# Kernel optimization log

Measured on AMD Instinct MI355X. Metric: run time of the kernel, lower is better.

The kernel has to match this reference:

```python
import jax, jax.numpy as jnp
import numpy as np

B, S, HID = 2, 2048, 2048
NH, NKV, HD = 16, 16, 128
SCALE = 1.0 / np.sqrt(HD)


def _rotate_half(x):
    x1, x2 = jnp.split(x, 2, axis=-1)
    return jnp.concatenate([-x2, x1], axis=-1)


def setup_inputs() -> dict:
    key = jax.random.key(0)
    k1, k2, k3 = jax.random.split(key, 3)
    hidden_states = jax.random.normal(k1, (B, S, HID), dtype=jnp.float32)
    # standard RoPE cos/sin tables, shape [S, HD]
    inv_freq = 1.0 / (10000.0 ** (np.arange(0, HD, 2, dtype=np.float32) / HD))
    freqs = np.outer(np.arange(S, dtype=np.float32), inv_freq)  # [S, HD/2]
    emb = np.concatenate([freqs, freqs], axis=-1)               # [S, HD]
    cos = jnp.asarray(np.cos(emb), dtype=jnp.float32)
    sin = jnp.asarray(np.sin(emb), dtype=jnp.float32)
    # torch Linear weights are [out, in]; forward computes x @ W.T
    w_qkv = jax.random.normal(k2, ((NH + 2 * NKV) * HD, HID), dtype=jnp.float32) * 0.02
    w_o = jax.random.normal(k3, (HID, NH * HD), dtype=jnp.float32) * 0.02
    return {"hidden_states": hidden_states, "cos": cos, "sin": sin,
            "w_qkv": w_qkv, "w_o": w_o}


def reference(hidden_states, cos, sin, w_qkv, w_o):
    b, s, _ = hidden_states.shape
    qkv = hidden_states @ w_qkv.T                         # [B,S,(NH+2*NKV)*HD]
    qkv = qkv.reshape(b, s, NH + 2 * NKV, HD)
    q = qkv[:, :, :NH]                                    # [B,S,NH,HD]
    k = qkv[:, :, NH:NH + NKV]                            # [B,S,NKV,HD]
    v = qkv[:, :, NH + NKV:]                              # [B,S,NKV,HD]
    # RoPE: broadcast cos/sin [S,HD] -> [1,S,1,HD]
    c = cos[None, :, None, :]
    sn = sin[None, :, None, :]
    q = q * c + _rotate_half(q) * sn
    k = k * c + _rotate_half(k) * sn
    scores = jnp.einsum("bihd,bjhd->bhij", q, k) * SCALE  # [B,H,S,S]
    attn = jax.nn.softmax(scores, axis=-1)
    out = jnp.einsum("bhij,bjhd->bihd", attn, v)          # [B,S,H,HD]
    out = out.reshape(b, s, NH * HD)
    return out @ w_o.T                                    # [B,S,HID]
```

## Files before the change

kernel.cpp:

```cpp
#include <hip/hip_runtime.h>
#include <hip/hip_bf16.h>

typedef float f32x4 __attribute__((ext_vector_type(4)));
typedef __bf16 bf16x8 __attribute__((ext_vector_type(8)));
typedef __bf16 bf16x4 __attribute__((ext_vector_type(4)));

#define S_LEN 2048
#define NHEADS 16
#define HDIM 128
#define KLOG2E (0.08838834764831845f * 1.4426950408889634f)
#define MSHIFT 2.0f

__device__ __forceinline__ void gld_lds16(const __bf16* g, __bf16* l) {
  __builtin_amdgcn_global_load_lds(
      (__attribute__((address_space(1))) void*)(void*)g,
      (__attribute__((address_space(3))) void*)l,
      16, 0, 0);
}

__global__ __launch_bounds__(256) void cvt_f32_bf16(const float* __restrict__ in,
                                                    __bf16* __restrict__ out, int n) {
  int i = (blockIdx.x * 256 + threadIdx.x) * 4;
  if (i >= n) return;
  float4 v = *(const float4*)(in + i);
  bf16x4 o;
  o[0] = (__bf16)v.x; o[1] = (__bf16)v.y; o[2] = (__bf16)v.z; o[3] = (__bf16)v.w;
  *(bf16x4*)(out + i) = o;
}


__global__ __launch_bounds__(256)
void gemm_bt_qkp(const __bf16* __restrict__ A, const __bf16* __restrict__ B,
                 __bf16* __restrict__ Qp, __bf16* __restrict__ Kp, int K) {
  __shared__ alignas(16) __bf16 As[128 * 32];
  __shared__ alignas(16) __bf16 Bs[128 * 32];
  const int tid = threadIdx.x;
  const int lane = tid & 63;
  const int w = tid >> 6;
  const int l15 = lane & 15, quad = lane >> 4;
  const int wm = w >> 1, wn = w & 1;
  const int am0 = blockIdx.y * 128;
  const int bn0 = blockIdx.x * 128;
  f32x4 acc[4][4] = {};
  const int c0 = tid, c1 = tid + 256;
  const int ar0 = c0 >> 2, ac0 = (c0 & 3) * 8;
  const int ar1 = c1 >> 2, ac1 = (c1 & 3) * 8;
  for (int k0 = 0; k0 < K; k0 += 32) {
    gld_lds16(A + (am0 + ar0) * K + k0 + ac0, As + c0 * 8);
    gld_lds16(A + (am0 + ar1) * K + k0 + ac1, As + c1 * 8);
    gld_lds16(B + (bn0 + ar0) * K + k0 + ac0, Bs + c0 * 8);
    gld_lds16(B + (bn0 + ar1) * K + k0 + ac1, Bs + c1 * 8);
    __syncthreads();
    bf16x8 af[4], bfr[4];
#pragma unroll
    for (int i = 0; i < 4; ++i)
      af[i] = *(const bf16x8*)(As + (wm * 64 + i * 16 + l15) * 32 + quad * 8);
#pragma unroll
    for (int i = 0; i < 4; ++i)
      bfr[i] = *(const bf16x8*)(Bs + (wn * 64 + i * 16 + l15) * 32 + quad * 8);
#pragma unroll
    for (int i = 0; i < 4; ++i)
#pragma unroll
      for (int j = 0; j < 4; ++j)
        acc[i][j] = __builtin_amdgcn_mfma_f32_16x16x32_bf16(af[i], bfr[j], acc[i][j], 0, 0, 0);
    __syncthreads();
  }
#pragma unroll
  for (int i = 0; i < 4; ++i) {
    const int row_b = am0 + wm * 64 + i * 16 + quad * 4;
    const int b = row_b >> 11;
    const int s = row_b & 2047;
    const int s16 = s >> 4;
    const int l15p0 = s & 15;
#pragma unroll
    for (int j = 0; j < 4; ++j) {
      const int col = bn0 + wn * 64 + j * 16 + l15;
      const int head = col >> 7;
      const int h = head & 15;
      const int d = col & 127;
      const int kk = d >> 5, quadp = (d >> 3) & 3, e = d & 7;
      __bf16* dst = (head < 16) ? Qp : Kp;
      size_t base = (((size_t)((b * 16 + h) * 128 + s16) * 4 + kk) * 64
                     + quadp * 16 + l15p0) * 8 + e;
#pragma unroll
      for (int r = 0; r < 4; ++r)
        dst[base + (size_t)r * 8] = (__bf16)acc[i][j][r];
    }
  }
}

__global__ __launch_bounds__(256)
void gemm_bt_vp(const __bf16* __restrict__ A, const __bf16* __restrict__ B,
                __bf16* __restrict__ Vp, int K) {
  __shared__ alignas(16) __bf16 As[128 * 32];
  __shared__ alignas(16) __bf16 Bs[128 * 32];
  const int tid = threadIdx.x;
  const int lane = tid & 63;
  const int w = tid >> 6;
  const int l15 = lane & 15, quad = lane >> 4;
  const int wm = w >> 1, wn = w & 1;
  const int am0 = blockIdx.y * 128;
  const int bn0 = blockIdx.x * 128;
  f32x4 acc[4][4] = {};
  const int c0 = tid, c1 = tid + 256;
  const int ar0 = c0 >> 2, ac0 = (c0 & 3) * 8;
  const int ar1 = c1 >> 2, ac1 = (c1 & 3) * 8;
  for (int k0 = 0; k0 < K; k0 += 32) {
    gld_lds16(A + (am0 + ar0) * K + k0 + ac0, As + c0 * 8);
    gld_lds16(A + (am0 + ar1) * K + k0 + ac1, As + c1 * 8);
    gld_lds16(B + (bn0 + ar0) * K + k0 + ac0, Bs + c0 * 8);
    gld_lds16(B + (bn0 + ar1) * K + k0 + ac1, Bs + c1 * 8);
    __syncthreads();
    bf16x8 af[4], bfr[4];
#pragma unroll
    for (int i = 0; i < 4; ++i)
      af[i] = *(const bf16x8*)(As + (wm * 64 + i * 16 + l15) * 32 + quad * 8);
#pragma unroll
    for (int i = 0; i < 4; ++i)
      bfr[i] = *(const bf16x8*)(Bs + (wn * 64 + i * 16 + l15) * 32 + quad * 8);
#pragma unroll
    for (int i = 0; i < 4; ++i)
#pragma unroll
      for (int j = 0; j < 4; ++j)
        acc[i][j] = __builtin_amdgcn_mfma_f32_16x16x32_bf16(af[i], bfr[j], acc[i][j], 0, 0, 0);
    __syncthreads();
  }
#pragma unroll
  for (int i = 0; i < 4; ++i) {
    const int row_b = am0 + wm * 64 + i * 16 + quad * 4;
    const int b = row_b >> 11;
    const int key0 = row_b & 2047;
    const int quadp = (key0 >> 3) & 3;
    const int kkv = key0 >> 5;
    const int e0 = key0 & 7;
#pragma unroll
    for (int j = 0; j < 4; ++j) {
      const int col = bn0 + wn * 64 + j * 16 + l15;
      const int h = col >> 7, dd = col & 127;
      const int tt = dd >> 4, l15p = dd & 15;
      bf16x4 o;
#pragma unroll
      for (int r = 0; r < 4; ++r) o[r] = (__bf16)acc[i][j][r];
      size_t addr = (((size_t)((b * 16 + h) * 8 + tt) * 64 + kkv) * 64
                     + quadp * 16 + l15p) * 8 + e0;
      *(bf16x4*)(Vp + addr) = o;
    }
  }
}

__global__ __launch_bounds__(256)
void rope_inplace(__bf16* __restrict__ Qp, __bf16* __restrict__ Kp,
                  const float* __restrict__ cosp, const float* __restrict__ sinp) {
  int t = blockIdx.x * 256 + threadIdx.x;
  int lane = t & 63;
  int kk = (t >> 6) & 1;
  int s16 = (t >> 7) & 127;
  int bh = (t >> 14) & 31;
  __bf16* buf = (t >> 19) ? Kp : Qp;
  int l15 = lane & 15, quad = lane >> 4;
  int s = s16 * 16 + l15;
  int d = kk * 32 + quad * 8;
  size_t base = (((size_t)(bh * 128 + s16) * 4 + kk) * 64 + lane) * 8;
  size_t base2 = base + 2 * 64 * 8;
  bf16x8 x1 = *(bf16x8*)(buf + base);
  bf16x8 x2 = *(bf16x8*)(buf + base2);
  float4 c0 = *(const float4*)(cosp + s * 128 + d);
  float4 c1 = *(const float4*)(cosp + s * 128 + d + 4);
  float4 s0 = *(const float4*)(sinp + s * 128 + d);
  float4 s1 = *(const float4*)(sinp + s * 128 + d + 4);
  float cs[8] = {c0.x, c0.y, c0.z, c0.w, c1.x, c1.y, c1.z, c1.w};
  float sn[8] = {s0.x, s0.y, s0.z, s0.w, s1.x, s1.y, s1.z, s1.w};
  bf16x8 o1, o2;
#pragma unroll
  for (int e = 0; e < 8; ++e) {
    float a = (float)x1[e], bb = (float)x2[e];
    o1[e] = (__bf16)(a * cs[e] - bb * sn[e]);
    o2[e] = (__bf16)(bb * cs[e] + a * sn[e]);
  }
  *(bf16x8*)(buf + base) = o1;
  *(bf16x8*)(buf + base2) = o2;
}

__global__ __launch_bounds__(256)
void gemm_bt_f(const __bf16* __restrict__ A, const __bf16* __restrict__ B,
               float* __restrict__ C, int M, int N, int K) {
  __shared__ alignas(16) __bf16 As[128 * 32];
  __shared__ alignas(16) __bf16 Bs[128 * 32];
  const int tid = threadIdx.x;
  const int lane = tid & 63;
  const int w = tid >> 6;
  const int l15 = lane & 15, quad = lane >> 4;
  const int wm = w >> 1, wn = w & 1;
  const int am0 = blockIdx.y * 128;
  const int bn0 = blockIdx.x * 128;
  f32x4 acc[4][4] = {};
  const int c0 = tid, c1 = tid + 256;
  const int ar0 = c0 >> 2, ac0 = (c0 & 3) * 8;
  const int ar1 = c1 >> 2, ac1 = (c1 & 3) * 8;
  for (int k0 = 0; k0 < K; k0 += 32) {
    gld_lds16(A + (am0 + ar0) * K + k0 + ac0, As + c0 * 8);
    gld_lds16(A + (am0 + ar1) * K + k0 + ac1, As + c1 * 8);
    gld_lds16(B + (bn0 + ar0) * K + k0 + ac0, Bs + c0 * 8);
    gld_lds16(B + (bn0 + ar1) * K + k0 + ac1, Bs + c1 * 8);
    __syncthreads();
    bf16x8 af[4], bfr[4];
#pragma unroll
    for (int i = 0; i < 4; ++i)
      af[i] = *(const bf16x8*)(As + (wm * 64 + i * 16 + l15) * 32 + quad * 8);
#pragma unroll
    for (int i = 0; i < 4; ++i)
      bfr[i] = *(const bf16x8*)(Bs + (wn * 64 + i * 16 + l15) * 32 + quad * 8);
#pragma unroll
    for (int i = 0; i < 4; ++i)
#pragma unroll
      for (int j = 0; j < 4; ++j)
        acc[i][j] = __builtin_amdgcn_mfma_f32_16x16x32_bf16(af[i], bfr[j], acc[i][j], 0, 0, 0);
    __syncthreads();
  }
#pragma unroll
  for (int i = 0; i < 4; ++i) {
    const int row_b = am0 + wm * 64 + i * 16 + quad * 4;
#pragma unroll
    for (int j = 0; j < 4; ++j) {
      const int col = bn0 + wn * 64 + j * 16 + l15;
#pragma unroll
      for (int r = 0; r < 4; ++r)
        C[(size_t)(row_b + r) * N + col] = acc[i][j][r];
    }
  }
}

__global__ __launch_bounds__(256)
void attn_kernel(const __bf16* __restrict__ Qp, const __bf16* __restrict__ Kp,
                 const __bf16* __restrict__ Vp, __bf16* __restrict__ O) {
  const int qt = blockIdx.x;
  const int bh = blockIdx.y;
  const int b = bh >> 4, h = bh & 15;
  const int tid = threadIdx.x;
  const int w = tid >> 6;
  const int lane = tid & 63;
  const int l15 = lane & 15, quad = lane >> 4;

  __shared__ alignas(16) __bf16 Kls[2][16 * 512];
  __shared__ alignas(16) __bf16 Vls[2][16 * 512];
  __shared__ alignas(16) __bf16 Ps[4][16][72];

  const __bf16* qbase = Qp + (size_t)bh * 262144 + lane * 8;
  const __bf16* kbase = Kp + (size_t)bh * 262144 + lane * 8;
  const __bf16* vbase = Vp + (size_t)bh * 262144 + lane * 8;

  bf16x8 qf[2][4];
#pragma unroll
  for (int qb = 0; qb < 2; ++qb)
#pragma unroll
    for (int kk = 0; kk < 4; ++kk)
      qf[qb][kk] = *(const bf16x8*)(qbase + (size_t)((qt * 8 + qb * 4 + w) * 4 + kk) * 512);

  bf16x8 onesf;
#pragma unroll
  for (int e = 0; e < 8; ++e) onesf[e] = (__bf16)1.0f;

  f32x4 o_acc[2][8] = {};
  f32x4 o_sum[2] = {};

#pragma unroll
  for (int ii = 0; ii < 4; ++ii) {
    const int c = w * 4 + ii;
    gld_lds16(kbase + (size_t)c * 512, &Kls[0][c * 512 + lane * 8]);
    gld_lds16(vbase + (size_t)((c >> 1) * 64 + (c & 1)) * 512,
              &Vls[0][c * 512 + lane * 8]);
  }
  __syncthreads();

  int cur = 0;
  for (int j0 = 0; j0 < S_LEN; j0 += 64) {
    if (j0 + 64 < S_LEN) {
      const int j16n = (j0 + 64) >> 4;
      const int kvn = (j0 + 64) >> 5;
#pragma unroll
      for (int ii = 0; ii < 4; ++ii) {
        const int c = w * 4 + ii;
        gld_lds16(kbase + (size_t)(j16n * 4 + c) * 512,
                  &Kls[cur ^ 1][c * 512 + lane * 8]);
        gld_lds16(vbase + (size_t)((c >> 1) * 64 + kvn + (c & 1)) * 512,
                  &Vls[cur ^ 1][c * 512 + lane * 8]);
      }
    }

    f32x4 sc[2][4] = {};
    __builtin_amdgcn_s_setprio(1);
#pragma unroll
    for (int kk = 0; kk < 4; ++kk) {
#pragma unroll
      for (int t = 0; t < 4; ++t) {
        bf16x8 kf = *(const bf16x8*)(&Kls[cur][(t * 4 + kk) * 512 + lane * 8]);
        sc[0][t] = __builtin_amdgcn_mfma_f32_16x16x32_bf16(qf[0][kk], kf, sc[0][t], 0, 0, 0);
        sc[1][t] = __builtin_amdgcn_mfma_f32_16x16x32_bf16(qf[1][kk], kf, sc[1][t], 0, 0, 0);
      }
    }
    __builtin_amdgcn_s_setprio(0);

    bf16x8 a[2][2];
#pragma unroll
    for (int qb = 0; qb < 2; ++qb) {
#pragma unroll
      for (int t = 0; t < 4; ++t)
#pragma unroll
        for (int r = 0; r < 4; ++r)
          Ps[w][quad * 4 + r][t * 16 + l15] =
              (__bf16)exp2f(sc[qb][t][r] * KLOG2E - MSHIFT);
      a[qb][0] = *(const bf16x8*)&Ps[w][l15][quad * 8];
      a[qb][1] = *(const bf16x8*)&Ps[w][l15][32 + quad * 8];
    }

    __builtin_amdgcn_s_setprio(1);
#pragma unroll
    for (int kk = 0; kk < 2; ++kk) {
      o_sum[0] = __builtin_amdgcn_mfma_f32_16x16x32_bf16(a[0][kk], onesf, o_sum[0], 0, 0, 0);
      o_sum[1] = __builtin_amdgcn_mfma_f32_16x16x32_bf16(a[1][kk], onesf, o_sum[1], 0, 0, 0);
#pragma unroll
      for (int t = 0; t < 8; ++t) {
        bf16x8 vf = *(const bf16x8*)(&Vls[cur][(t * 2 + kk) * 512 + lane * 8]);
        o_acc[0][t] = __builtin_amdgcn_mfma_f32_16x16x32_bf16(a[0][kk], vf, o_acc[0][t], 0, 0, 0);
        o_acc[1][t] = __builtin_amdgcn_mfma_f32_16x16x32_bf16(a[1][kk], vf, o_acc[1][t], 0, 0, 0);
      }
    }
    __builtin_amdgcn_s_setprio(0);

    __syncthreads();
    cur ^= 1;
  }

#pragma unroll
  for (int qb = 0; qb < 2; ++qb) {
    float inv[4];
#pragma unroll
    for (int r = 0; r < 4; ++r) inv[r] = 1.0f / o_sum[qb][r];
    const int row0 = qt * 128 + (qb * 4 + w) * 16 + quad * 4;
#pragma unroll
    for (int t = 0; t < 8; ++t)
#pragma unroll
      for (int r = 0; r < 4; ++r)
        O[(size_t)(b * S_LEN + row0 + r) * 2048 + h * HDIM + t * 16 + l15] =
            (__bf16)(o_acc[qb][t][r] * inv[r]);
  }
}

extern "C" void kernel_launch(void* const* d_in, const int* in_sizes, int n_in,
                              void* d_out, int out_size, void* d_ws, size_t ws_size,
                              hipStream_t stream) {
  const float* hs   = (const float*)d_in[0];
  const float* cosp = (const float*)d_in[1];
  const float* sinp = (const float*)d_in[2];
  const float* wqkv = (const float*)d_in[3];
  const float* wo   = (const float*)d_in[4];
  float* out = (float*)d_out;

  char* ws = (char*)d_ws;
  __bf16* Xb   = (__bf16*)(ws);
  __bf16* Obuf = (__bf16*)(ws);
  __bf16* Wqb  = (__bf16*)(ws + 16777216);
  __bf16* Wob  = (__bf16*)(ws + 41943040);
  __bf16* Qp   = (__bf16*)(ws + 50331648);
  __bf16* Kp   = (__bf16*)(ws + 67108864);
  __bf16* Vp   = (__bf16*)(ws + 83886080);
  if (ws_size < 100663296) return;

  cvt_f32_bf16<<<8192, 256, 0, stream>>>(hs, Xb, 8388608);
  cvt_f32_bf16<<<12288, 256, 0, stream>>>(wqkv, Wqb, 12582912);
  cvt_f32_bf16<<<4096, 256, 0, stream>>>(wo, Wob, 4194304);

  gemm_bt_qkp<<<dim3(32, 32), 256, 0, stream>>>(Xb, Wqb, Qp, Kp, 2048);
  gemm_bt_vp<<<dim3(16, 32), 256, 0, stream>>>(Xb, Wqb + 8388608, Vp, 2048);
  rope_inplace<<<4096, 256, 0, stream>>>(Qp, Kp, cosp, sinp);
  attn_kernel<<<dim3(16, 32), 256, 0, stream>>>(Qp, Kp, Vp, Obuf);
  gemm_bt_f<<<dim3(16, 32), 256, 0, stream>>>(Obuf, Wob, out, 4096, 2048, 2048);
}
```

Measured before the change: 464.8 us.

## Rewrite projection GEMMs with 4-stage async LDS pipeline and larger 512-thread tiles

Replaces the three projection GEMMs with a shared templated core. It runs a 4-slot LDS ring, prefetching three k-steps ahead with global_load_lds and explicit vmcnt waits, so it needs one barrier per step instead of two. Tiles grow to 256x256 (QK) or 128x256 (V, output) with 8 waves per block, and setprio is raised around the MFMA bursts. The goal is to hide global-load latency and raise reuse per block. The costs are fewer blocks for the 256-CU part and more LDS use per block.

```diff
diff --git a/kernel.cpp b/kernel.cpp
--- a/kernel.cpp
+++ b/kernel.cpp
@@ -16,6 +16,15 @@
       (__attribute__((address_space(1))) void*)(void*)g,
       (__attribute__((address_space(3))) void*)l,
       16, 0, 0);
+}
+
+template <int N>
+__device__ __forceinline__ void waitv() {
+  if constexpr (N == 8)      asm volatile("s_waitcnt vmcnt(8)" ::: "memory");
+  else if constexpr (N == 6) asm volatile("s_waitcnt vmcnt(6)" ::: "memory");
+  else if constexpr (N == 4) asm volatile("s_waitcnt vmcnt(4)" ::: "memory");
+  else if constexpr (N == 3) asm volatile("s_waitcnt vmcnt(3)" ::: "memory");
+  else                       asm volatile("s_waitcnt vmcnt(0)" ::: "memory");
 }
 
 __global__ __launch_bounds__(256) void cvt_f32_bf16(const float* __restrict__ in,
@@ -28,46 +37,90 @@
   *(bf16x4*)(out + i) = o;
 }
 
-
-__global__ __launch_bounds__(256)
+template <int MREP>
+__device__ __forceinline__ void gemm_core(const __bf16* __restrict__ A,
+                                          const __bf16* __restrict__ B,
+                                          __bf16* lds, int am0, int bn0,
+                                          f32x4 (&acc)[MREP][4]) {
+  constexpr int K = 2048;
+  constexpr int AF = MREP * 2;
+  constexpr int SLOT = (AF + 16) * 512;
+  constexpr int NA = AF / 8;
+  constexpr int NL = NA + 2;
+  const int tid = threadIdx.x;
+  const int w = tid >> 6, lane = tid & 63;
+  const int l15 = lane & 15;
+  const int wm = w >> 2, wn = w & 3;
+
+  const __bf16* asrc = A + (size_t)(am0 + l15) * K + (lane >> 4) * 8;
+  const __bf16* bsrc = B + (size_t)(bn0 + l15) * K + (lane >> 4) * 8;
+
+  auto stage = [&](int t) {
+    __bf16* s = lds + (t & 3) * SLOT;
+#pragma unroll
+    for (int i = 0; i < NA; ++i) {
+      const int f = w * NA + i;
+      gld_lds16(asrc + (size_t)f * (16 * K) + t * 32, s + f * 512 + lane * 8);
+    }
+#pragma unroll
+    for (int i = 0; i < 2; ++i) {
+      const int g = w * 2 + i;
+      gld_lds16(bsrc + (size_t)g * (16 * K) + t * 32, s + (AF + g) * 512 + lane * 8);
+    }
+  };
+
+  stage(0); stage(1); stage(2);
+  waitv<2 * NL>();
+  __builtin_amdgcn_s_barrier();
+
+  for (int t = 0; t < 64; ++t) {
+    if (t < 61) stage(t + 3);
+    const __bf16* s = lds + (t & 3) * SLOT + lane * 8;
+    const __bf16* sB = s + AF * 512;
+    bf16x8 bfr[4];
+#pragma unroll
+    for (int j = 0; j < 4; ++j)
+      bfr[j] = *(const bf16x8*)(sB + (wn * 4 + j) * 512);
+#pragma unroll
+    for (int half = 0; half < MREP / 4; ++half) {
+      bf16x8 af[4];
+#pragma unroll
+      for (int i = 0; i < 4; ++i)
+        af[i] = *(const bf16x8*)(s + (wm * MREP + half * 4 + i) * 512);
+      __builtin_amdgcn_s_setprio(1);
+#pragma unroll
+      for (int i = 0; i < 4; ++i)
+#pragma unroll
+        for (int j = 0; j < 4; ++j)
+          acc[half * 4 + i][j] = __builtin_amdgcn_mfma_f32_16x16x32_bf16(
+              af[i], bfr[j], acc[half * 4 + i][j], 0, 0, 0);
+      __builtin_amdgcn_s_setprio(0);
+    }
+    if (t < 63) {
+      if (t < 61)      waitv<2 * NL>();
+      else if (t == 61) waitv<NL>();
+      else             waitv<0>();
+      __builtin_amdgcn_s_barrier();
+    }
+  }
+}
+
+
+__global__ __launch_bounds__(512)
 void gemm_bt_qkp(const __bf16* __restrict__ A, const __bf16* __restrict__ B,
-                 __bf16* __restrict__ Qp, __bf16* __restrict__ Kp, int K) {
-  __shared__ alignas(16) __bf16 As[128 * 32];
-  __shared__ alignas(16) __bf16 Bs[128 * 32];
-  const int tid = threadIdx.x;
-  const int lane = tid & 63;
-  const int w = tid >> 6;
+                 __bf16* __restrict__ Qp, __bf16* __restrict__ Kp) {
+  __shared__ alignas(16) __bf16 lds[4 * 32 * 512];
+  const int am0 = blockIdx.y * 256;
+  const int bn0 = blockIdx.x * 256;
+  const int tid = threadIdx.x;
+  const int w = tid >> 6, lane = tid & 63;
   const int l15 = lane & 15, quad = lane >> 4;
-  const int wm = w >> 1, wn = w & 1;
-  const int am0 = blockIdx.y * 128;
-  const int bn0 = blockIdx.x * 128;
-  f32x4 acc[4][4] = {};
-  const int c0 = tid, c1 = tid + 256;
-  const int ar0 = c0 >> 2, ac0 = (c0 & 3) * 8;
-  const int ar1 = c1 >> 2, ac1 = (c1 & 3) * 8;
-  for (int k0 = 0; k0 < K; k0 += 32) {
-    gld_lds16(A + (am0 + ar0) * K + k0 + ac0, As + c0 * 8);
-    gld_lds16(A + (am0 + ar1) * K + k0 + ac1, As + c1 * 8);
-    gld_lds16(B + (bn0 + ar0) * K + k0 + ac0, Bs + c0 * 8);
-    gld_lds16(B + (bn0 + ar1) * K + k0 + ac1, Bs + c1 * 8);
-    __syncthreads();
-    bf16x8 af[4], bfr[4];
-#pragma unroll
-    for (int i = 0; i < 4; ++i)
-      af[i] = *(const bf16x8*)(As + (wm * 64 + i * 16 + l15) * 32 + quad * 8);
-#pragma unroll
-    for (int i = 0; i < 4; ++i)
-      bfr[i] = *(const bf16x8*)(Bs + (wn * 64 + i * 16 + l15) * 32 + quad * 8);
-#pragma unroll
-    for (int i = 0; i < 4; ++i)
-#pragma unroll
-      for (int j = 0; j < 4; ++j)
-        acc[i][j] = __builtin_amdgcn_mfma_f32_16x16x32_bf16(af[i], bfr[j], acc[i][j], 0, 0, 0);
-    __syncthreads();
-  }
-#pragma unroll
-  for (int i = 0; i < 4; ++i) {
-    const int row_b = am0 + wm * 64 + i * 16 + quad * 4;
+  const int wm = w >> 2, wn = w & 3;
+  f32x4 acc[8][4] = {};
+  gemm_core<8>(A, B, lds, am0, bn0, acc);
+#pragma unroll
+  for (int i = 0; i < 8; ++i) {
+    const int row_b = am0 + wm * 128 + i * 16 + quad * 4;
     const int b = row_b >> 11;
     const int s = row_b & 2047;
     const int s16 = s >> 4;
@@ -89,42 +142,18 @@
   }
 }
 
-__global__ __launch_bounds__(256)
+__global__ __launch_bounds__(512)
 void gemm_bt_vp(const __bf16* __restrict__ A, const __bf16* __restrict__ B,
-                __bf16* __restrict__ Vp, int K) {
-  __shared__ alignas(16) __bf16 As[128 * 32];
-  __shared__ alignas(16) __bf16 Bs[128 * 32];
-  const int tid = threadIdx.x;
-  const int lane = tid & 63;
-  const int w = tid >> 6;
+                __bf16* __restrict__ Vp) {
+  __shared__ alignas(16) __bf16 lds[4 * 24 * 512];
+  const int am0 = blockIdx.y * 128;
+  const int bn0 = blockIdx.x * 256;
+  const int tid = threadIdx.x;
+  const int w = tid >> 6, lane = tid & 63;
   const int l15 = lane & 15, quad = lane >> 4;
-  const int wm = w >> 1, wn = w & 1;
-  const int am0 = blockIdx.y * 128;
-  const int bn0 = blockIdx.x * 128;
+  const int wm = w >> 2, wn = w & 3;
   f32x4 acc[4][4] = {};
-  const int c0 = tid, c1 = tid + 256;
-  const int ar0 = c0 >> 2, ac0 = (c0 & 3) * 8;
-  const int ar1 = c1 >> 2, ac1 = (c1 & 3) * 8;
-  for (int k0 = 0; k0 < K; k0 += 32) {
-    gld_lds16(A + (am0 + ar0) * K + k0 + ac0, As + c0 * 8);
-    gld_lds16(A + (am0 + ar1) * K + k0 + ac1, As + c1 * 8);
-    gld_lds16(B + (bn0 + ar0) * K + k0 + ac0, Bs + c0 * 8);
-    gld_lds16(B + (bn0 + ar1) * K + k0 + ac1, Bs + c1 * 8);
-    __syncthreads();
-    bf16x8 af[4], bfr[4];
-#pragma unroll
-    for (int i = 0; i < 4; ++i)
-      af[i] = *(const bf16x8*)(As + (wm * 64 + i * 16 + l15) * 32 + quad * 8);
-#pragma unroll
-    for (int i = 0; i < 4; ++i)
-      bfr[i] = *(const bf16x8*)(Bs + (wn * 64 + i * 16 + l15) * 32 + quad * 8);
-#pragma unroll
-    for (int i = 0; i < 4; ++i)
-#pragma unroll
-      for (int j = 0; j < 4; ++j)
-        acc[i][j] = __builtin_amdgcn_mfma_f32_16x16x32_bf16(af[i], bfr[j], acc[i][j], 0, 0, 0);
-    __syncthreads();
-  }
+  gemm_core<4>(A, B, lds, am0, bn0, acc);
 #pragma unroll
   for (int i = 0; i < 4; ++i) {
     const int row_b = am0 + wm * 64 + i * 16 + quad * 4;
@@ -144,6 +173,31 @@
       size_t addr = (((size_t)((b * 16 + h) * 8 + tt) * 64 + kkv) * 64
                      + quadp * 16 + l15p) * 8 + e0;
       *(bf16x4*)(Vp + addr) = o;
+    }
+  }
+}
+
+__global__ __launch_bounds__(512)
+void gemm_bt_f(const __bf16* __restrict__ A, const __bf16* __restrict__ B,
+               float* __restrict__ C) {
+  __shared__ alignas(16) __bf16 lds[4 * 24 * 512];
+  const int am0 = blockIdx.y * 128;
+  const int bn0 = blockIdx.x * 256;
+  const int tid = threadIdx.x;
+  const int w = tid >> 6, lane = tid & 63;
+  const int l15 = lane & 15, quad = lane >> 4;
+  const int wm = w >> 2, wn = w & 3;
+  f32x4 acc[4][4] = {};
+  gemm_core<4>(A, B, lds, am0, bn0, acc);
+#pragma unroll
+  for (int i = 0; i < 4; ++i) {
+    const int row_b = am0 + wm * 64 + i * 16 + quad * 4;
+#pragma unroll
+    for (int j = 0; j < 4; ++j) {
+      const int col = bn0 + wn * 64 + j * 16 + l15;
+#pragma unroll
+      for (int r = 0; r < 4; ++r)
+        C[(size_t)(row_b + r) * 2048 + col] = acc[i][j][r];
     }
   }
 }
@@ -182,55 +236,6 @@
 }
 
 __global__ __launch_bounds__(256)
-void gemm_bt_f(const __bf16* __restrict__ A, const __bf16* __restrict__ B,
-               float* __restrict__ C, int M, int N, int K) {
-  __shared__ alignas(16) __bf16 As[128 * 32];
-  __shared__ alignas(16) __bf16 Bs[128 * 32];
-  const int tid = threadIdx.x;
-  const int lane = tid & 63;
-  const int w = tid >> 6;
-  const int l15 = lane & 15, quad = lane >> 4;
-  const int wm = w >> 1, wn = w & 1;
-  const int am0 = blockIdx.y * 128;
-  const int bn0 = blockIdx.x * 128;
-  f32x4 acc[4][4] = {};
-  const int c0 = tid, c1 = tid + 256;
-  const int ar0 = c0 >> 2, ac0 = (c0 & 3) * 8;
-  const int ar1 = c1 >> 2, ac1 = (c1 & 3) * 8;
-  for (int k0 = 0; k0 < K; k0 += 32) {
-    gld_lds16(A + (am0 + ar0) * K + k0 + ac0, As + c0 * 8);
-    gld_lds16(A + (am0 + ar1) * K + k0 + ac1, As + c1 * 8);
-    gld_lds16(B + (bn0 + ar0) * K + k0 + ac0, Bs + c0 * 8);
-    gld_lds16(B + (bn0 + ar1) * K + k0 + ac1, Bs + c1 * 8);
-    __syncthreads();
-    bf16x8 af[4], bfr[4];
-#pragma unroll
-    for (int i = 0; i < 4; ++i)
-      af[i] = *(const bf16x8*)(As + (wm * 64 + i * 16 + l15) * 32 + quad * 8);
-#pragma unroll
-    for (int i = 0; i < 4; ++i)
-      bfr[i] = *(const bf16x8*)(Bs + (wn * 64 + i * 16 + l15) * 32 + quad * 8);
-#pragma unroll
-    for (int i = 0; i < 4; ++i)
-#pragma unroll
-      for (int j = 0; j < 4; ++j)
-        acc[i][j] = __builtin_amdgcn_mfma_f32_16x16x32_bf16(af[i], bfr[j], acc[i][j], 0, 0, 0);
-    __syncthreads();
-  }
-#pragma unroll
-  for (int i = 0; i < 4; ++i) {
-    const int row_b = am0 + wm * 64 + i * 16 + quad * 4;
-#pragma unroll
-    for (int j = 0; j < 4; ++j) {
-      const int col = bn0 + wn * 64 + j * 16 + l15;
-#pragma unroll
-      for (int r = 0; r < 4; ++r)
-        C[(size_t)(row_b + r) * N + col] = acc[i][j][r];
-    }
-  }
-}
-
-__global__ __launch_bounds__(256)
 void attn_kernel(const __bf16* __restrict__ Qp, const __bf16* __restrict__ Kp,
                  const __bf16* __restrict__ Vp, __bf16* __restrict__ O) {
   const int qt = blockIdx.x;
@@ -370,9 +375,9 @@
   cvt_f32_bf16<<<12288, 256, 0, stream>>>(wqkv, Wqb, 12582912);
   cvt_f32_bf16<<<4096, 256, 0, stream>>>(wo, Wob, 4194304);
 
-  gemm_bt_qkp<<<dim3(32, 32), 256, 0, stream>>>(Xb, Wqb, Qp, Kp, 2048);
-  gemm_bt_vp<<<dim3(16, 32), 256, 0, stream>>>(Xb, Wqb + 8388608, Vp, 2048);
+  gemm_bt_qkp<<<dim3(16, 16), 512, 0, stream>>>(Xb, Wqb, Qp, Kp);
+  gemm_bt_vp<<<dim3(8, 32), 512, 0, stream>>>(Xb, Wqb + 8388608, Vp);
   rope_inplace<<<4096, 256, 0, stream>>>(Qp, Kp, cosp, sinp);
   attn_kernel<<<dim3(16, 32), 256, 0, stream>>>(Qp, Kp, Vp, Obuf);
-  gemm_bt_f<<<dim3(16, 32), 256, 0, stream>>>(Obuf, Wob, out, 4096, 2048, 2048);
-}
+  gemm_bt_f<<<dim3(8, 32), 512, 0, stream>>>(Obuf, Wob, out);
+}
```

After: 435.7 us. -6.3%, faster.
